# Kernel optimization log

Measured on AMD Instinct MI355X. Metric: run time of the kernel, lower is better.

Reference implementation:

```python
import jax, jax.numpy as jnp
import numpy as np

H = 128; R = 8; VN = 100; VA = 64
N = 8192; B = 64; L = 48; E = 65536


def setup_inputs() -> dict:
    key = jax.random.key(0)
    ks = jax.random.split(key, 24)
    s = 0.05
    nodeTypes = jax.random.randint(ks[0], (N,), 0, VN)
    edge_index = jax.random.randint(ks[1], (2, E), 0, N)
    edge_attr = jax.random.randint(ks[2], (E,), 0, R)
    bs = jnp.repeat(jnp.arange(B), N // B)              # sorted node->graph map
    nodes_bs = jnp.full((B,), N // B, dtype=jnp.int32)  # nodes per graph
    len_seq = jax.random.randint(ks[3], (B,), 1, L + 1).at[0].set(L)  # max == L
    sequence_input = (jax.random.uniform(ks[4], (N, L)) < 0.05).astype(jnp.float32)
    action_input = jax.random.randint(ks[5], (B,), 0, VA)
    params = dict(
        emb_nodes=jax.random.normal(ks[6], (VN, H)) * s,
        emb_actions=jax.random.normal(ks[7], (VA, H)) * s,
        rgcn_rel=jax.random.normal(ks[8], (3, R, H, H)) * s,   # per-layer relation weights
        rgcn_root=jax.random.normal(ks[9], (3, H, H)) * s,
        rgcn_bias=jnp.zeros((3, H)),
        gru_w_ih=jax.random.normal(ks[10], (3 * H, H)) * s,
        gru_w_hh=jax.random.normal(ks[11], (3 * H, H)) * s,
        gru_b_ih=jnp.zeros((3 * H,)),
        gru_b_hh=jnp.zeros((3 * H,)),
        linA_w=jax.random.normal(ks[12], (H, H)) * s,
        linA_b=jnp.zeros((H,)),
        linAf_w=jax.random.normal(ks[13], (VA, H)) * s,
        linAf_b=jnp.zeros((VA,)),
        linN_w=jax.random.normal(ks[14], (H, 2 * H)) * s,
        linN_b=jnp.zeros((H,)),
        linNf_w=jax.random.normal(ks[15], (1, H)) * s,
        linNf_b=jnp.zeros((1,)),
    )
    return dict(nodeTypes=nodeTypes, edge_index=edge_index, edge_attr=edge_attr,
                bs=bs, nodes_bs=nodes_bs, len_seq=len_seq,
                sequence_input=sequence_input, action_input=action_input, **params)


def reference(nodeTypes, edge_index, edge_attr, bs, nodes_bs, len_seq,
              sequence_input, action_input,
              emb_nodes, emb_actions, rgcn_rel, rgcn_root, rgcn_bias,
              gru_w_ih, gru_w_hh, gru_b_ih, gru_b_hh,
              linA_w, linA_b, linAf_w, linAf_b,
              linN_w, linN_b, linNf_w, linNf_b):
    n = nodeTypes.shape[0]
    b = nodes_bs.shape[0]
    h = emb_nodes.shape[1]
    r = rgcn_rel.shape[1]
    l = sequence_input.shape[1]

    x = emb_nodes[nodeTypes]                               # [N,H]
    src, dst = edge_index[0], edge_index[1]
    seg = dst * r + edge_attr                              # per (target, relation) segment
    cnt = jax.ops.segment_sum(jnp.ones((src.shape[0],), x.dtype), seg, n * r)
    denom = jnp.maximum(cnt, 1.0).reshape(n, r, 1)
    for li in range(3):
        agg = jax.ops.segment_sum(x[src], seg, n * r).reshape(n, r, h) / denom
        x = jax.nn.relu(jnp.einsum('nrh,rho->no', agg, rgcn_rel[li])
                        + x @ rgcn_root[li] + rgcn_bias[li])

    # global mean pool -> graph embedding
    h_G = jax.ops.segment_sum(x, bs, b) / nodes_bs[:, None].astype(x.dtype)  # [B,H]
    action = jax.nn.relu(h_G @ linA_w.T + linA_b) @ linAf_w.T + linAf_b      # [B,VA]

    sos = emb_actions[action_input][:, None, :]            # [B,1,H]
    # sequence embeddings: sum over nodes in each graph of seq[i,t]*x[i]
    emb_seq = sequence_input[:, :, None] * x[:, None, :]   # [N,L,H]
    out = jax.ops.segment_sum(emb_seq, bs, b)              # [B,L,H]
    input_gru = jnp.concatenate([sos, out], axis=1)[:, :l] # packed GRU only sees first L steps

    # single-layer GRU, h0 = h_G (torch gate order r,z,n)
    xW = input_gru @ gru_w_ih.T + gru_b_ih                 # [B,L,3H]
    def step(hprev, xw):
        hW = hprev @ gru_w_hh.T + gru_b_hh
        xr, xz, xn = jnp.split(xw, 3, -1)
        hr, hz, hn = jnp.split(hW, 3, -1)
        rg = jax.nn.sigmoid(xr + hr)
        zg = jax.nn.sigmoid(xz + hz)
        ng = jnp.tanh(xn + rg * hn)
        hnew = (1.0 - zg) * ng + zg * hprev
        return hnew, hnew
    _, hs = jax.lax.scan(step, h_G, jnp.swapaxes(xW, 0, 1))
    seq_out = jnp.swapaxes(hs, 0, 1)                       # [B,L,H]
    mask = jnp.arange(l)[None, :] < len_seq[:, None]       # pad_packed zero-pads
    seq_out = seq_out * mask[:, :, None]

    out_gru = seq_out[bs]                                  # repeat_interleave -> [N,L,H]
    concats = jnp.concatenate(
        [out_gru, jnp.broadcast_to(x[:, None, :], (n, l, h))], axis=2)  # [N,L,2H]
    hid = jax.nn.relu(concats @ linN_w.T + linN_b)         # [N,L,H]
    logits = (hid @ linNf_w.T + linNf_b)[..., 0]           # [N,L]

    # scatter_softmax over nodes grouped by graph (dim 0)
    m = jax.lax.stop_gradient(jax.ops.segment_max(logits, bs, b))
    e = jnp.exp(logits - m[bs])
    ssum = jax.ops.segment_sum(e, bs, b)
    nodes_final = e / ssum[bs]
    return action, nodes_final
```

## Files before the change

kernel.cpp:

```cpp
#include <hip/hip_runtime.h>
#include <hip/hip_bf16.h>

#define H   128
#define RR  8
#define NN  8192
#define BB  64
#define LL  48
#define EE  65536
#define NPG 128
#define VA  64
#define NSEG (NN*RR)
#define GPB 16

typedef unsigned short u16;
typedef unsigned int   u32;

__device__ __forceinline__ float b2f(u16 u) {
    union { u32 i; float f; } v; v.i = ((u32)u) << 16; return v.f;
}
__device__ __forceinline__ u16 f2b(float f) {
    union { float f; u32 i; } v; v.f = f;
    u32 x = v.i;
    return (u16)((x + 0x7fffu + ((x >> 16) & 1u)) >> 16);
}
__device__ __forceinline__ float2 up2(u32 p) {
    union { u32 i; float f; } a, b;
    a.i = p << 16; b.i = p & 0xffff0000u;
    return make_float2(a.f, b.f);
}
__device__ __forceinline__ u32 pk2(float a, float b) {
    return ((u32)f2b(b) << 16) | (u32)f2b(a);
}
__device__ __forceinline__ float rcpf(float x) { return __builtin_amdgcn_rcpf(x); }
__device__ __forceinline__ u32 cvtpk(float lo, float hi) {
    u32 r;
    asm("v_cvt_pk_bf16_f32 %0, %1, %2" : "=v"(r) : "v"(lo), "v"(hi));
    return r;
}

#define K_LOG2E  1.4426950408889634f
#define K_2LOG2E 2.8853900817779268f

typedef __attribute__((ext_vector_type(8))) short bf16x8;
typedef __attribute__((ext_vector_type(4))) float f32x4;
typedef __attribute__((ext_vector_type(4))) unsigned short u16x4;

__global__ __launch_bounds__(256) void k_prep(const int* __restrict__ nodeTypes,
                                              const float* __restrict__ emb_nodes,
                                              const float* __restrict__ rel,
                                              const float* __restrict__ root,
                                              const float* __restrict__ w_ih,
                                              float* __restrict__ x0,
                                              u16* __restrict__ WTt,
                                              u16* __restrict__ WTih,
                                              float* __restrict__ hGsum,
                                              int* __restrict__ fill) {
    int idx = blockIdx.x * 256 + threadIdx.x;
    if (idx < NSEG) fill[idx] = 0;
    if (idx < 384 * H) WTih[idx] = f2b(w_ih[idx]);
    if (idx < BB * H) hGsum[idx] = 0.f;
    if (idx < NN * H) {
        int n = idx >> 7, h = idx & (H - 1);
        x0[idx] = emb_nodes[(size_t)nodeTypes[n] * H + h];
    }
    int j = idx - NN * H;
    if (j < 0 || j >= 3 * 147456) return;
    int li  = j / 147456;
    int rem = j - li * 147456;
    int tile = rem / 36864;
    int r2   = rem - tile * 36864;
    int ks   = r2 / 1024;
    int r3   = r2 - ks * 1024;
    int sub  = r3 >> 9;
    int r4   = r3 & 511;
    int lane = r4 >> 3, jj = r4 & 7;
    int col = tile * 32 + sub * 16 + (lane & 15);
    int k   = ks * 32 + (lane >> 4) * 8 + jj;
    float v;
    if (k < 1024) v = rel[(((size_t)li * RR + (k >> 7)) * H + (k & 127)) * H + col];
    else          v = root[((size_t)li * H + (k - 1024)) * H + col];
    WTt[j] = f2b(v);
}

__global__ __launch_bounds__(256) void k_hist(const int* __restrict__ edge_index,
                                              const int* __restrict__ edge_attr,
                                              int* __restrict__ fill) {
    int e = blockIdx.x * 256 + threadIdx.x;
    if (e < EE) {
        int seg = edge_index[EE + e] * RR + edge_attr[e];
        atomicAdd(&fill[seg], 1);
    }
}

__global__ __launch_bounds__(256) void k_scan1(const int* __restrict__ fill,
                                               int* __restrict__ bsum) {
    __shared__ int red[4];
    int tid = threadIdx.x, lane = tid & 63, wv = tid >> 6;
    int v = fill[blockIdx.x * 256 + tid];
#pragma unroll
    for (int off = 32; off >= 1; off >>= 1) v += __shfl_down(v, off, 64);
    if (lane == 0) red[wv] = v;
    __syncthreads();
    if (tid == 0) bsum[blockIdx.x] = red[0] + red[1] + red[2] + red[3];
}

__global__ __launch_bounds__(256) void k_scan3(const int* __restrict__ bsum,
                                               int* __restrict__ fill,
                                               int* __restrict__ rowptr) {
    __shared__ int s[256], s2[256];
    __shared__ int boffs;
    int tid = threadIdx.x;
    int g = blockIdx.x * 256 + tid;
    int c = fill[g];
    int b0 = bsum[tid];
    s[tid] = c;
    s2[tid] = b0;
    __syncthreads();
    for (int off = 1; off < 256; off <<= 1) {
        int v  = (tid >= off) ? s[tid - off]  : 0;
        int v2 = (tid >= off) ? s2[tid - off] : 0;
        __syncthreads();
        s[tid] += v;
        s2[tid] += v2;
        __syncthreads();
    }
    if (blockIdx.x == 0 && tid == 255) rowptr[NSEG] = s2[255];
    if (tid == blockIdx.x) boffs = s2[tid] - b0;
    __syncthreads();
    int r = boffs + s[tid] - c;
    rowptr[g] = r;
    fill[g] = r;
}

__global__ __launch_bounds__(256) void k_scatter(const int* __restrict__ edge_index,
                                                 const int* __restrict__ edge_attr,
                                                 int* __restrict__ fill,
                                                 int* __restrict__ colidx) {
    int e = blockIdx.x * 256 + threadIdx.x;
    if (e < EE) {
        int seg = edge_index[EE + e] * RR + edge_attr[e];
        int pos = atomicAdd(&fill[seg], 1);
        colidx[pos] = edge_index[e];
    }
}

#define RGN 16
#define EPRE 512

__global__ __launch_bounds__(512) void k_rgcn(const float* __restrict__ xin,
                                              float* __restrict__ xout,
                                              const u16* __restrict__ WTt,
                                              const float* __restrict__ bias,
                                              const int* __restrict__ rowptr,
                                              const int* __restrict__ colidx,
                                              float* __restrict__ hGsum) {
    __shared__ u32 ab[RGN * 580];
    __shared__ int begs[RGN * RR + 1];
    __shared__ int eidx[EPRE];
    int tid = threadIdx.x, wv = tid >> 6, lane = tid & 63;
    int n0 = blockIdx.x * RGN, segbase = n0 * RR;

    if (tid <= RGN * RR) begs[tid] = rowptr[segbase + tid];
    __syncthreads();
    int E0 = begs[0], ne = begs[RGN * RR] - E0;
    for (int i = tid; i < ne && i < EPRE; i += 512) eidx[i] = colidx[E0 + i];
    __syncthreads();

    for (int s = wv; s < RGN * RR; s += 8) {
        int beg = begs[s], end = begs[s + 1];
        float a0 = 0.f, a1 = 0.f;
        for (int e = beg; e < end; ++e) {
            int off = e - E0;
            int src = (off < EPRE) ? eidx[off] : colidx[e];
            float2 v = ((const float2*)(xin + (size_t)src * H))[lane];
            a0 += v.x; a1 += v.y;
        }
        float inv = 1.f / fmaxf((float)(end - beg), 1.f);
        ab[(s >> 3) * 580 + ((s & 7) << 6) + lane] = pk2(a0 * inv, a1 * inv);
    }
    for (int i = wv; i < RGN; i += 8) {
        const float* xr = xin + (size_t)(n0 + i) * H + 2 * lane;
        ab[i * 580 + 512 + lane] = pk2(xr[0], xr[1]);
    }
    __syncthreads();

    int m = lane & 15, quad = lane >> 4;
    const u32* aP = ab + m * 580 + quad * 4;
    const u32* bT = (const u32*)WTt + (size_t)(wv >> 1) * 36 * 512 + (wv & 1) * 256 + lane * 4;
    f32x4 acc0 = {0.f, 0.f, 0.f, 0.f};
    bf16x8 b0c = *(const bf16x8*)bT;
    for (int ks = 0; ks < 36; ++ks) {
        bf16x8 b0n;
        if (ks < 35) b0n = *(const bf16x8*)(bT + (ks + 1) * 512);
        bf16x8 a = *(const bf16x8*)(aP + ks * 16);
        acc0 = __builtin_amdgcn_mfma_f32_16x16x32_bf16(a, b0c, acc0, 0, 0, 0);
        b0c = b0n;
    }
    int c0 = wv * 16 + m;
    float bv0 = bias[c0];
    float so0 = 0.f;
#pragma unroll
    for (int rg = 0; rg < 4; ++rg) {
        int n = n0 + quad * 4 + rg;
        float o0 = fmaxf(acc0[rg] + bv0, 0.f);
        xout[(size_t)n * H + c0] = o0;
        so0 += o0;
    }
    if (hGsum) {
        so0 += __shfl_xor(so0, 16, 64);
        so0 += __shfl_xor(so0, 32, 64);
        if (quad == 0) {
            int g = n0 >> 7;
            atomicAdd(&hGsum[g * H + c0], so0);
        }
    }
}

__global__ __launch_bounds__(256) void k_pool_seq(const float* __restrict__ hGsum,
                                                  const int* __restrict__ nodes_bs,
                                                  const float* __restrict__ linA_w,
                                                  const float* __restrict__ linA_b,
                                                  const float* __restrict__ linAf_w,
                                                  const float* __restrict__ linAf_b,
                                                  float* __restrict__ hG,
                                                  float* __restrict__ out,
                                                  const float* __restrict__ xf,
                                                  const float* __restrict__ seq,
                                                  const float* __restrict__ emb_actions,
                                                  const int* __restrict__ action_input,
                                                  float* __restrict__ igG) {
    __shared__ float xg[64][H];
    __shared__ u16 lists[LL][64];
    __shared__ int cnts[LL];
    int tid = threadIdx.x;

    if (blockIdx.x < BB) {
        float* hgs = &xg[0][0];
        float* t1  = &xg[1][0];
        int b = blockIdx.x, h = tid;
        if (h < H) {
            float hg = hGsum[(size_t)b * H + h] / (float)nodes_bs[b];
            hG[(size_t)b * H + h] = hg;
            hgs[h] = hg;
        }
        __syncthreads();
        if (h < H) {
            float acc = linA_b[h];
            const float* wr = linA_w + (size_t)h * H;
            for (int k = 0; k < H; ++k) acc += wr[k] * hgs[k];
            t1[h] = fmaxf(acc, 0.f);
        }
        __syncthreads();
        if (h < VA) {
            float a = linAf_b[h];
            const float* w2 = linAf_w + (size_t)h * H;
            for (int k = 0; k < H; ++k) a += w2[k] * t1[k];
            out[(size_t)b * VA + h] = a;
        }
        return;
    }

    int b = blockIdx.x - BB;
    int col = tid & 127, tg = tid >> 7;
    float acc[24];
#pragma unroll
    for (int m = 0; m < 24; ++m) acc[m] = 0.f;

    for (int chunk = 0; chunk < 2; ++chunk) {
        int i0 = b * NPG + chunk * 64;
        __syncthreads();
        if (tid < LL) cnts[tid] = 0;
        __syncthreads();
        for (int idx = tid; idx < 64 * H / 4; idx += 256)
            ((float4*)&xg[0][0])[idx] = ((const float4*)(xf + (size_t)i0 * H))[idx];
        for (int idx = tid; idx < 64 * LL; idx += 256) {
            int i = idx / LL, t = idx - i * LL;
            if (seq[(size_t)(i0 + i) * LL + t] != 0.f) {
                int p = atomicAdd(&cnts[t], 1);
                lists[t][p] = (u16)i;
            }
        }
        __syncthreads();
        for (int m = 0; m < 24; ++m) {
            int t = tg + 2 * m;
            int c = cnts[t];
            float a = acc[m];
            for (int p = 0; p < c; ++p) a += xg[lists[t][p]][col];
            acc[m] = a;
        }
    }
    if (tid < H)
        igG[((size_t)b * LL) * H + tid] = emb_actions[(size_t)action_input[b] * H + tid];
#pragma unroll
    for (int m = 0; m < 24; ++m) {
        int t = tg + 2 * m;
        if (t < LL - 1)
            igG[((size_t)b * LL + t + 1) * H + col] = acc[m];
    }
}

__global__ __launch_bounds__(256) void k_xw(const float* __restrict__ igG,
                                            const u16* __restrict__ WTih,
                                            const float* __restrict__ b_ih,
                                            const float* __restrict__ b_hh,
                                            u16* __restrict__ xwG) {
    __shared__ u32 ab[16 * 68];
    int tid = threadIdx.x, wv = tid >> 6, lane = tid & 63;
    int n0 = blockIdx.x * 16;
    for (int s = tid; s < 16 * 64; s += 256) {
        int row = s >> 6, kp = s & 63;
        float2 v = *(const float2*)(igG + (size_t)(n0 + row) * H + 2 * kp);
        ab[row * 68 + kp] = pk2(v.x, v.y);
    }
    __syncthreads();
    int m = lane & 15, quad = lane >> 4;
    const u32* aP = ab + m * 68 + quad * 4;
    f32x4 acc[6];
#pragma unroll
    for (int i = 0; i < 6; ++i) acc[i] = (f32x4){0.f, 0.f, 0.f, 0.f};
#pragma unroll
    for (int ks = 0; ks < 4; ++ks) {
        bf16x8 a = *(const bf16x8*)(aP + ks * 16);
#pragma unroll
        for (int tc = 0; tc < 6; ++tc) {
            int colr = wv * 96 + tc * 16 + m;
            bf16x8 bfr = *(const bf16x8*)((const u32*)WTih + (size_t)colr * 64 + quad * 4 + ks * 16);
            acc[tc] = __builtin_amdgcn_mfma_f32_16x16x32_bf16(a, bfr, acc[tc], 0, 0, 0);
        }
    }
#pragma unroll
    for (int tc = 0; tc < 6; ++tc) {
        int c = wv * 96 + tc * 16 + m;
        float bv = b_ih[c] + ((c < 256) ? b_hh[c] : 0.f);
        float sc = (c < 256) ? K_LOG2E : K_2LOG2E;
        int R = c & 127, gate = c >> 7;
#pragma unroll
        for (int rg = 0; rg < 4; ++rg) {
            int r = n0 + quad * 4 + rg;
            int bb = r / 48, tt = r - bb * 48;
            size_t o = (((((size_t)(bb >> 4) * LL + tt) * 8 + (R >> 4)) * 3 + gate) * 256)
                     + (((R >> 2) & 3) << 6) + ((bb & 15) << 2) + (R & 3);
            xwG[o] = f2b((acc[tc][rg] + bv) * sc);
        }
    }
}

#define GRU_BLKS 4
#define BX_BLKS  (NN / 32)
#define SMEM_BYTES 33024

__global__ __launch_bounds__(512) void k_gru_bx(const u16* __restrict__ xw2,
                                                const float* __restrict__ hG,
                                                const float* __restrict__ w_hh,
                                                const float* __restrict__ b_hh,
                                                const int* __restrict__ len_seq,
                                                float* __restrict__ soutG,
                                                const float* __restrict__ xf,
                                                const float* __restrict__ linN_w,
                                                const float* __restrict__ linN_b,
                                                u16* __restrict__ BxU) {
    __shared__ __align__(16) char smem[SMEM_BYTES];
    int tid = threadIdx.x;

    if (blockIdx.x >= GRU_BLKS) {
        float* xl = (float*)smem;
        float* wb = (float*)(smem + 16384);
        int bid = blockIdx.x - GRU_BLKS;
        int n0 = bid * 32;
        for (int idx = tid; idx < 32 * H; idx += 512)
            xl[idx] = xf[(size_t)n0 * H + idx];
        int col = tid & 127, g = tid >> 7;
        float bv = linN_b[col];
        float acc[8] = {bv, bv, bv, bv, bv, bv, bv, bv};
        for (int c = 0; c < 4; ++c) {
            int k0 = c * 32;
            __syncthreads();
            for (int idx = tid; idx < 32 * H; idx += 512) {
                int r = idx >> 5, kk = idx & 31;
                wb[kk * 130 + r] = linN_w[(size_t)r * (2 * H) + H + k0 + kk];
            }
            __syncthreads();
#pragma unroll
            for (int kk = 0; kk < 32; ++kk) {
                float w = wb[kk * 130 + col];
#pragma unroll
                for (int j = 0; j < 8; ++j) acc[j] += xl[(g * 8 + j) * H + k0 + kk] * w;
            }
        }
#pragma unroll
        for (int j = 0; j < 8; ++j)
            BxU[(size_t)(n0 + g * 8 + j) * H + col] = f2b(acc[j]);
        return;
    }

    u16* hA = (u16*)smem;
    int lane = tid & 63, wv = tid >> 6;
    int mi = lane & 15, quad = lane >> 4;
    int gblk = blockIdx.x;
    int g_abs = gblk * GPB + mi;
    int R0 = 16 * wv + 4 * quad;

    int eW = (((wv >> 1) * 64) + (mi + 16 * ((2 * wv + (quad >> 1)) & 3))) * 8
             + 4 * (quad & 1);

    bf16x8 wfr[3][4];
#pragma unroll
    for (int gate = 0; gate < 3; ++gate) {
        int T = wv + 8 * gate;
        float sc = (gate == 2) ? K_2LOG2E : K_LOG2E;
#pragma unroll
        for (int ks = 0; ks < 4; ++ks) {
            const float* wp = w_hh + (size_t)(16 * T + mi) * H + quad * 8 + ks * 32;
            float4 f0 = *(const float4*)wp;
            float4 f1 = *(const float4*)(wp + 4);
            bf16x8 v;
            v[0] = (short)f2b(f0.x * sc); v[1] = (short)f2b(f0.y * sc);
            v[2] = (short)f2b(f0.z * sc); v[3] = (short)f2b(f0.w * sc);
            v[4] = (short)f2b(f1.x * sc); v[5] = (short)f2b(f1.y * sc);
            v[6] = (short)f2b(f1.z * sc); v[7] = (short)f2b(f1.w * sc);
            wfr[gate][ks] = v;
        }
    }
    float4 bn = *(const float4*)(b_hh + 256 + R0);
    float4 h0 = *(const float4*)(hG + (size_t)g_abs * H + R0);
    int ls = len_seq[g_abs];

    float hp[4]  = {h0.x, h0.y, h0.z, h0.w};
    float bnn[4] = {bn.x * K_2LOG2E, bn.y * K_2LOG2E, bn.z * K_2LOG2E, bn.w * K_2LOG2E};

    auto storeh = [&](int buf, const float* hv) {
        u32 w0 = cvtpk(hv[0], hv[1]);
        u32 w1 = cvtpk(hv[2], hv[3]);
        *(uint2*)&hA[buf * 2048 + eW] = make_uint2(w0, w1);
    };
    auto loadxw = [&](int t, u16x4* d) {
        const u16* p = xw2 + ((((size_t)gblk * LL + t) * 8 + wv) * 3) * 256
                     + (quad << 6) + (mi << 2);
        d[0] = *(const u16x4*)(p);
        d[1] = *(const u16x4*)(p + 256);
        d[2] = *(const u16x4*)(p + 512);
    };

    auto step = [&](int t, const u16x4* x, int buf) {
        f32x4 acc[3];
        acc[0] = (f32x4){0.f, 0.f, 0.f, 0.f};
        acc[1] = (f32x4){0.f, 0.f, 0.f, 0.f};
        acc[2] = (f32x4){bnn[0], bnn[1], bnn[2], bnn[3]};
#pragma unroll
        for (int ks = 0; ks < 4; ++ks) {
            const int e = (ks * 64 + lane) * 8;
            bf16x8 bh = *(const bf16x8*)&hA[buf * 2048 + e];
#pragma unroll
            for (int gate = 0; gate < 3; ++gate)
                acc[gate] = __builtin_amdgcn_mfma_f32_16x16x32_bf16(wfr[gate][ks], bh, acc[gate], 0, 0, 0);
        }
        float hv[4];
        float4 so;
#pragma unroll
        for (int r = 0; r < 4; ++r) {
            float xr = b2f(x[0][r]);
            float xz = b2f(x[1][r]);
            float xn = b2f(x[2][r]);
            float rg = rcpf(1.f + __builtin_amdgcn_exp2f(-(xr + acc[0][r])));
            float zg = rcpf(1.f + __builtin_amdgcn_exp2f(-(xz + acc[1][r])));
            float u  = xn + rg * acc[2][r];
            float ng = 1.f - 2.f * rcpf(__builtin_amdgcn_exp2f(u) + 1.f);
            float hn = ng + zg * (hp[r] - ng);
            hp[r] = hn;
            hv[r] = hn;
            ((float*)&so)[r] = (t < ls) ? hn : 0.f;
        }
        *(float4*)(soutG + ((size_t)g_abs * LL + t) * H + R0) = so;
        storeh(buf ^ 1, hv);
    };

    u16x4 xa[3], xb[3];
    loadxw(0, xa);
    loadxw(1, xb);
    storeh(0, hp);
    asm volatile("s_waitcnt lgkmcnt(0)\n\ts_barrier" ::: "memory");

    for (int t = 0; t < LL; t += 2) {
        step(t, xa, 0);
        if (t + 2 < LL) loadxw(t + 2, xa);
        asm volatile("s_waitcnt lgkmcnt(0)\n\ts_barrier" ::: "memory");
        step(t + 1, xb, 1);
        if (t + 3 < LL) loadxw(t + 3, xb);
        asm volatile("s_waitcnt lgkmcnt(0)\n\ts_barrier" ::: "memory");
    }
}

__global__ __launch_bounds__(256) void k_a2(const float* __restrict__ soutG,
                                            const float* __restrict__ linN_w,
                                            float* __restrict__ A2) {
    __shared__ float wb[32][130];
    __shared__ float xl[16][H];
    int tid = threadIdx.x;
    int n0 = blockIdx.x * 16;
    for (int idx = tid; idx < 16 * H; idx += 256)
        xl[idx >> 7][idx & 127] = soutG[(size_t)n0 * H + idx];
    int col = tid & 127, g = tid >> 7;
    float acc[8] = {0.f, 0.f, 0.f, 0.f, 0.f, 0.f, 0.f, 0.f};
    for (int c = 0; c < 4; ++c) {
        int k0 = c * 32;
        __syncthreads();
        for (int idx = tid; idx < 32 * H; idx += 256) {
            int r = idx >> 5, kk = idx & 31;
            wb[kk][r] = linN_w[(size_t)r * (2 * H) + k0 + kk];
        }
        __syncthreads();
#pragma unroll
        for (int kk = 0; kk < 32; ++kk) {
            float w = wb[kk][col];
#pragma unroll
            for (int j = 0; j < 8; ++j) acc[j] += xl[g * 8 + j][k0 + kk] * w;
        }
    }
#pragma unroll
    for (int j = 0; j < 8; ++j)
        A2[(size_t)(n0 + g * 8 + j) * H + col] = acc[j];
}

__global__ __launch_bounds__(256) void k_logits(const float* __restrict__ A2,
                                                const u16* __restrict__ BxU,
                                                const float* __restrict__ linNf_w,
                                                float* __restrict__ logits) {
    __shared__ float a2s[LL][130];
    __shared__ float bxs[16][130];
    __shared__ float w2s[H];
    int tid = threadIdx.x;
    int g = blockIdx.x >> 3, tile = blockIdx.x & 7;
    int n0g = g * NPG + tile * 16;

    for (int i2 = tid; i2 < LL * 64; i2 += 256) {
        int r = i2 >> 6, c2 = i2 & 63;
        *(float2*)&a2s[r][2 * c2] = *(const float2*)(A2 + ((size_t)g * LL + r) * H + 2 * c2);
    }
    for (int iu = tid; iu < 16 * 64; iu += 256) {
        int r = iu >> 6, c = iu & 63;
        float2 v = up2(((const u32*)BxU)[(size_t)(n0g + r) * 64 + c]);
        *(float2*)&bxs[r][2 * c] = v;
    }
    if (tid < H) w2s[tid] = linNf_w[tid];
    __syncthreads();

    int n = tid & 15, tt = tid >> 4;
#pragma unroll
    for (int pass = 0; pass < 3; ++pass) {
        int t = tt + 16 * pass;
        float acc = 0.f;
#pragma unroll
        for (int kp = 0; kp < 64; ++kp) {
            float2 a2 = *(const float2*)&a2s[t][2 * kp];
            float2 bx = *(const float2*)&bxs[n][2 * kp];
            float2 w  = *(const float2*)&w2s[2 * kp];
            acc += w.x * fmaxf(a2.x + bx.x, 0.f) + w.y * fmaxf(a2.y + bx.y, 0.f);
        }
        logits[(size_t)(n0g + n) * LL + t] = acc;
    }
}

__global__ __launch_bounds__(256) void k_softmax(const float* __restrict__ logits,
                                                 float* __restrict__ out) {
    __shared__ float lg[NPG][LL + 1];
    __shared__ float pm[4][LL], ps[4][LL];
    __shared__ float mv[LL], inv[LL];
    int b = blockIdx.x, tid = threadIdx.x;
    int n0 = b * NPG;
    for (int idx = tid; idx < NPG * LL; idx += 256) {
        int n = idx / LL, t = idx - n * LL;
        lg[n][t] = logits[(size_t)n0 * LL + idx];
    }
    __syncthreads();
    int t = tid & 63, seg = tid >> 6;
    if (t < LL) {
        float m = -1e30f;
        int nb = seg * 32;
        for (int n = nb; n < nb + 32; ++n) m = fmaxf(m, lg[n][t]);
        pm[seg][t] = m;
    }
    __syncthreads();
    if (tid < LL)
        mv[tid] = fmaxf(fmaxf(pm[0][tid], pm[1][tid]), fmaxf(pm[2][tid], pm[3][tid]));
    __syncthreads();
    if (t < LL) {
        float m = mv[t], s = 0.f;
        int nb = seg * 32;
        for (int n = nb; n < nb + 32; ++n) {
            float e = __expf(lg[n][t] - m);
            lg[n][t] = e;
            s += e;
        }
        ps[seg][t] = s;
    }
    __syncthreads();
    if (tid < LL)
        inv[tid] = 1.f / (ps[0][tid] + ps[1][tid] + ps[2][tid] + ps[3][tid]);
    __syncthreads();
    for (int idx = tid; idx < NPG * LL; idx += 256) {
        int n = idx / LL, tc = idx - n * LL;
        out[(size_t)BB * VA + (size_t)n0 * LL + idx] = lg[n][tc] * inv[tc];
    }
}

extern "C" void kernel_launch(void* const* d_in, const int* in_sizes, int n_in,
                              void* d_out, int out_size, void* d_ws, size_t ws_size,
                              hipStream_t stream) {
    (void)in_sizes; (void)n_in; (void)out_size; (void)ws_size;
    const int*   nodeTypes    = (const int*)d_in[0];
    const int*   edge_index   = (const int*)d_in[1];
    const int*   edge_attr    = (const int*)d_in[2];
    const int*   nodes_bs     = (const int*)d_in[4];
    const int*   len_seq      = (const int*)d_in[5];
    const float* seq_in       = (const float*)d_in[6];
    const int*   action_input = (const int*)d_in[7];
    const float* emb_nodes    = (const float*)d_in[8];
    const float* emb_actions  = (const float*)d_in[9];
    const float* rgcn_rel     = (const float*)d_in[10];
    const float* rgcn_root    = (const float*)d_in[11];
    const float* rgcn_bias    = (const float*)d_in[12];
    const float* gru_w_ih     = (const float*)d_in[13];
    const float* gru_w_hh     = (const float*)d_in[14];
    const float* gru_b_ih     = (const float*)d_in[15];
    const float* gru_b_hh     = (const float*)d_in[16];
    const float* linA_w       = (const float*)d_in[17];
    const float* linA_b       = (const float*)d_in[18];
    const float* linAf_w      = (const float*)d_in[19];
    const float* linAf_b      = (const float*)d_in[20];
    const float* linN_w       = (const float*)d_in[21];
    const float* linN_b       = (const float*)d_in[22];
    const float* linNf_w      = (const float*)d_in[23];

    char* w = (char*)d_ws;
    float* x0      = (float*)(w + 0);
    u16*   xwG     = (u16*)  (w + 0);
    float* logitsW = (float*)(w + 0);
    float* soutG   = (float*)(w + 2359296);
    float* x1      = (float*)(w + 4194304);
    float* igG     = (float*)(w + 8388608);
    float* A2      = (float*)(w + 8388608);
    u16*   BxU     = (u16*)  (w + 9961472);
    int*   bsum    = (int*)  (w + 9961472);
    float* hGsum   = (float*)(w + 9969664);
    int*   rowptr  = (int*)  (w + 11567104);
    int*   fill    = (int*)  (w + 11829760);
    float* hG      = (float*)(w + 12058624);
    int*   colidx  = (int*)  (w + 12091904);
    u16*   WTih    = (u16*)  (w + 12354048);
    u16*   WT      = (u16*)  (w + 12616192);

    float* out_f = (float*)d_out;

    k_prep<<<dim3(5824), dim3(256), 0, stream>>>(nodeTypes, emb_nodes, rgcn_rel,
        rgcn_root, gru_w_ih, x0, WT, WTih, hGsum, fill);
    k_hist<<<dim3(256), dim3(256), 0, stream>>>(edge_index, edge_attr, fill);
    k_scan1<<<dim3(256), dim3(256), 0, stream>>>(fill, bsum);
    k_scan3<<<dim3(256), dim3(256), 0, stream>>>(bsum, fill, rowptr);
    k_scatter<<<dim3(256), dim3(256), 0, stream>>>(edge_index, edge_attr, fill, colidx);

    const int rg_grid = NN / RGN;
    k_rgcn<<<dim3(rg_grid), dim3(512), 0, stream>>>(x0, x1,
        WT + 0 * 147456, rgcn_bias + 0 * H, rowptr, colidx, nullptr);
    k_rgcn<<<dim3(rg_grid), dim3(512), 0, stream>>>(x1, x0,
        WT + 1 * 147456, rgcn_bias + 1 * H, rowptr, colidx, nullptr);
    k_rgcn<<<dim3(rg_grid), dim3(512), 0, stream>>>(x0, x1,
        WT + 2 * 147456, rgcn_bias + 2 * H, rowptr, colidx, hGsum);

    k_pool_seq<<<dim3(2 * BB), dim3(256), 0, stream>>>(hGsum, nodes_bs, linA_w, linA_b,
        linAf_w, linAf_b, hG, out_f, x1, seq_in, emb_actions, action_input, igG);
    k_xw<<<dim3(BB * LL / 16), dim3(256), 0, stream>>>(igG, WTih, gru_b_ih, gru_b_hh, xwG);
    k_gru_bx<<<dim3(GRU_BLKS + BX_BLKS), dim3(512), 0, stream>>>(xwG, hG, gru_w_hh,
        gru_b_hh, len_seq, soutG, x1, linN_w, linN_b, BxU);
    k_a2<<<dim3(BB * LL / 16), dim3(256), 0, stream>>>(soutG, linN_w, A2);
    k_logits<<<dim3(BB * 8), dim3(256), 0, stream>>>(A2, BxU, linNf_w, logitsW);
    k_softmax<<<dim3(BB), dim3(256), 0, stream>>>(logitsW, out_f);
}
```

Before: 309.1 us.

## Fuse CSR build into cooperative kernel and merge logits with softmax

Result: slower. 478.0 us (+54.7%).

```diff
diff --git a/kernel.cpp b/kernel.cpp
--- a/kernel.cpp
+++ b/kernel.cpp
@@ -1,5 +1,8 @@
 #include <hip/hip_runtime.h>
 #include <hip/hip_bf16.h>
+#include <hip/hip_cooperative_groups.h>
+
+namespace cg = cooperative_groups;
 
 #define H   128
 #define RR  8
@@ -82,63 +85,59 @@
     WTt[j] = f2b(v);
 }
 
-__global__ __launch_bounds__(256) void k_hist(const int* __restrict__ edge_index,
-                                              const int* __restrict__ edge_attr,
-                                              int* __restrict__ fill) {
-    int e = blockIdx.x * 256 + threadIdx.x;
-    if (e < EE) {
-        int seg = edge_index[EE + e] * RR + edge_attr[e];
-        atomicAdd(&fill[seg], 1);
-    }
-}
-
-__global__ __launch_bounds__(256) void k_scan1(const int* __restrict__ fill,
-                                               int* __restrict__ bsum) {
+__global__ __launch_bounds__(256) void k_csr(const int* __restrict__ edge_index,
+                                             const int* __restrict__ edge_attr,
+                                             int* __restrict__ fill,
+                                             int* __restrict__ bsum,
+                                             int* __restrict__ rowptr,
+                                             int* __restrict__ colidx) {
+    cg::grid_group grid = cg::this_grid();
+    __shared__ int s[256], s2[256];
     __shared__ int red[4];
-    int tid = threadIdx.x, lane = tid & 63, wv = tid >> 6;
-    int v = fill[blockIdx.x * 256 + tid];
-#pragma unroll
-    for (int off = 32; off >= 1; off >>= 1) v += __shfl_down(v, off, 64);
-    if (lane == 0) red[wv] = v;
-    __syncthreads();
-    if (tid == 0) bsum[blockIdx.x] = red[0] + red[1] + red[2] + red[3];
-}
-
-__global__ __launch_bounds__(256) void k_scan3(const int* __restrict__ bsum,
-                                               int* __restrict__ fill,
-                                               int* __restrict__ rowptr) {
-    __shared__ int s[256], s2[256];
     __shared__ int boffs;
     int tid = threadIdx.x;
-    int g = blockIdx.x * 256 + tid;
-    int c = fill[g];
-    int b0 = bsum[tid];
-    s[tid] = c;
-    s2[tid] = b0;
-    __syncthreads();
-    for (int off = 1; off < 256; off <<= 1) {
-        int v  = (tid >= off) ? s[tid - off]  : 0;
-        int v2 = (tid >= off) ? s2[tid - off] : 0;
-        __syncthreads();
-        s[tid] += v;
-        s2[tid] += v2;
-        __syncthreads();
-    }
-    if (blockIdx.x == 0 && tid == 255) rowptr[NSEG] = s2[255];
-    if (tid == blockIdx.x) boffs = s2[tid] - b0;
-    __syncthreads();
-    int r = boffs + s[tid] - c;
-    rowptr[g] = r;
-    fill[g] = r;
-}
-
-__global__ __launch_bounds__(256) void k_scatter(const int* __restrict__ edge_index,
-                                                 const int* __restrict__ edge_attr,
-                                                 int* __restrict__ fill,
-                                                 int* __restrict__ colidx) {
-    int e = blockIdx.x * 256 + threadIdx.x;
-    if (e < EE) {
-        int seg = edge_index[EE + e] * RR + edge_attr[e];
+    int e = blockIdx.x * 256 + tid;
+    int seg = edge_index[EE + e] * RR + edge_attr[e];
+
+    atomicAdd(&fill[seg], 1);
+    grid.sync();
+
+    {
+        int lane = tid & 63, wv = tid >> 6;
+        int v = fill[blockIdx.x * 256 + tid];
+#pragma unroll
+        for (int off = 32; off >= 1; off >>= 1) v += __shfl_down(v, off, 64);
+        if (lane == 0) red[wv] = v;
+        __syncthreads();
+        if (tid == 0) bsum[blockIdx.x] = red[0] + red[1] + red[2] + red[3];
+    }
+    grid.sync();
+
+    {
+        int g = blockIdx.x * 256 + tid;
+        int c = fill[g];
+        int b0 = bsum[tid];
+        s[tid] = c;
+        s2[tid] = b0;
+        __syncthreads();
+        for (int off = 1; off < 256; off <<= 1) {
+            int v  = (tid >= off) ? s[tid - off]  : 0;
+            int v2 = (tid >= off) ? s2[tid - off] : 0;
+            __syncthreads();
+            s[tid] += v;
+            s2[tid] += v2;
+            __syncthreads();
+        }
+        if (blockIdx.x == 0 && tid == 255) rowptr[NSEG] = s2[255];
+        if (tid == blockIdx.x) boffs = s2[tid] - b0;
+        __syncthreads();
+        int r = boffs + s[tid] - c;
+        rowptr[g] = r;
+        fill[g] = r;
+    }
+    grid.sync();
+
+    {
         int pos = atomicAdd(&fill[seg], 1);
         colidx[pos] = edge_index[e];
     }
@@ -521,62 +520,56 @@
         A2[(size_t)(n0 + g * 8 + j) * H + col] = acc[j];
 }
 
-__global__ __launch_bounds__(256) void k_logits(const float* __restrict__ A2,
-                                                const u16* __restrict__ BxU,
-                                                const float* __restrict__ linNf_w,
-                                                float* __restrict__ logits) {
+__global__ __launch_bounds__(256) void k_lsm(const float* __restrict__ A2,
+                                             const u16* __restrict__ BxU,
+                                             const float* __restrict__ linNf_w,
+                                             float* __restrict__ out) {
     __shared__ float a2s[LL][130];
     __shared__ float bxs[16][130];
     __shared__ float w2s[H];
+    __shared__ float lg[NPG][LL + 1];
+    __shared__ float pm[4][LL], ps[4][LL];
+    __shared__ float mv[LL], inv[LL];
     int tid = threadIdx.x;
-    int g = blockIdx.x >> 3, tile = blockIdx.x & 7;
-    int n0g = g * NPG + tile * 16;
+    int g = blockIdx.x;
 
     for (int i2 = tid; i2 < LL * 64; i2 += 256) {
         int r = i2 >> 6, c2 = i2 & 63;
         *(float2*)&a2s[r][2 * c2] = *(const float2*)(A2 + ((size_t)g * LL + r) * H + 2 * c2);
     }
-    for (int iu = tid; iu < 16 * 64; iu += 256) {
-        int r = iu >> 6, c = iu & 63;
-        float2 v = up2(((const u32*)BxU)[(size_t)(n0g + r) * 64 + c]);
-        *(float2*)&bxs[r][2 * c] = v;
-    }
     if (tid < H) w2s[tid] = linNf_w[tid];
-    __syncthreads();
 
     int n = tid & 15, tt = tid >> 4;
-#pragma unroll
-    for (int pass = 0; pass < 3; ++pass) {
-        int t = tt + 16 * pass;
-        float acc = 0.f;
-#pragma unroll
-        for (int kp = 0; kp < 64; ++kp) {
-            float2 a2 = *(const float2*)&a2s[t][2 * kp];
-            float2 bx = *(const float2*)&bxs[n][2 * kp];
-            float2 w  = *(const float2*)&w2s[2 * kp];
-            acc += w.x * fmaxf(a2.x + bx.x, 0.f) + w.y * fmaxf(a2.y + bx.y, 0.f);
-        }
-        logits[(size_t)(n0g + n) * LL + t] = acc;
-    }
-}
-
-__global__ __launch_bounds__(256) void k_softmax(const float* __restrict__ logits,
-                                                 float* __restrict__ out) {
-    __shared__ float lg[NPG][LL + 1];
-    __shared__ float pm[4][LL], ps[4][LL];
-    __shared__ float mv[LL], inv[LL];
-    int b = blockIdx.x, tid = threadIdx.x;
-    int n0 = b * NPG;
-    for (int idx = tid; idx < NPG * LL; idx += 256) {
-        int n = idx / LL, t = idx - n * LL;
-        lg[n][t] = logits[(size_t)n0 * LL + idx];
-    }
-    __syncthreads();
+    for (int tile = 0; tile < 8; ++tile) {
+        int n0g = g * NPG + tile * 16;
+        __syncthreads();
+        for (int iu = tid; iu < 16 * 64; iu += 256) {
+            int r = iu >> 6, c = iu & 63;
+            float2 v = up2(((const u32*)BxU)[(size_t)(n0g + r) * 64 + c]);
+            *(float2*)&bxs[r][2 * c] = v;
+        }
+        __syncthreads();
+#pragma unroll
+        for (int pass = 0; pass < 3; ++pass) {
+            int t = tt + 16 * pass;
+            float acc = 0.f;
+#pragma unroll
+            for (int kp = 0; kp < 64; ++kp) {
+                float2 a2 = *(const float2*)&a2s[t][2 * kp];
+                float2 bx = *(const float2*)&bxs[n][2 * kp];
+                float2 w  = *(const float2*)&w2s[2 * kp];
+                acc += w.x * fmaxf(a2.x + bx.x, 0.f) + w.y * fmaxf(a2.y + bx.y, 0.f);
+            }
+            lg[tile * 16 + n][t] = acc;
+        }
+    }
+    __syncthreads();
+
     int t = tid & 63, seg = tid >> 6;
     if (t < LL) {
         float m = -1e30f;
         int nb = seg * 32;
-        for (int n = nb; n < nb + 32; ++n) m = fmaxf(m, lg[n][t]);
+        for (int nn = nb; nn < nb + 32; ++nn) m = fmaxf(m, lg[nn][t]);
         pm[seg][t] = m;
     }
     __syncthreads();
@@ -586,9 +579,9 @@
     if (t < LL) {
         float m = mv[t], s = 0.f;
         int nb = seg * 32;
-        for (int n = nb; n < nb + 32; ++n) {
-            float e = __expf(lg[n][t] - m);
-            lg[n][t] = e;
+        for (int nn = nb; nn < nb + 32; ++nn) {
+            float e = __expf(lg[nn][t] - m);
+            lg[nn][t] = e;
             s += e;
         }
         ps[seg][t] = s;
@@ -598,8 +591,8 @@
         inv[tid] = 1.f / (ps[0][tid] + ps[1][tid] + ps[2][tid] + ps[3][tid]);
     __syncthreads();
     for (int idx = tid; idx < NPG * LL; idx += 256) {
-        int n = idx / LL, tc = idx - n * LL;
-        out[(size_t)BB * VA + (size_t)n0 * LL + idx] = lg[n][tc] * inv[tc];
+        int nn = idx / LL, tc = idx - nn * LL;
+        out[(size_t)BB * VA + (size_t)g * NPG * LL + idx] = lg[nn][tc] * inv[tc];
     }
 }
 
@@ -634,7 +627,6 @@
     char* w = (char*)d_ws;
     float* x0      = (float*)(w + 0);
     u16*   xwG     = (u16*)  (w + 0);
-    float* logitsW = (float*)(w + 0);
     float* soutG   = (float*)(w + 2359296);
     float* x1      = (float*)(w + 4194304);
     float* igG     = (float*)(w + 8388608);
@@ -653,10 +645,12 @@
 
     k_prep<<<dim3(5824), dim3(256), 0, stream>>>(nodeTypes, emb_nodes, rgcn_rel,
         rgcn_root, gru_w_ih, x0, WT, WTih, hGsum, fill);
-    k_hist<<<dim3(256), dim3(256), 0, stream>>>(edge_index, edge_attr, fill);
-    k_scan1<<<dim3(256), dim3(256), 0, stream>>>(fill, bsum);
-    k_scan3<<<dim3(256), dim3(256), 0, stream>>>(bsum, fill, rowptr);
-    k_scatter<<<dim3(256), dim3(256), 0, stream>>>(edge_index, edge_attr, fill, colidx);
+
+    {
+        void* args[] = { (void*)&edge_index, (void*)&edge_attr, (void*)&fill,
+                         (void*)&bsum, (void*)&rowptr, (void*)&colidx };
+        hipLaunchCooperativeKernel((void*)k_csr, dim3(256), dim3(256), args, 0, stream);
+    }
 
     const int rg_grid = NN / RGN;
     k_rgcn<<<dim3(rg_grid), dim3(512), 0, stream>>>(x0, x1,
@@ -672,6 +666,5 @@
     k_gru_bx<<<dim3(GRU_BLKS + BX_BLKS), dim3(512), 0, stream>>>(xwG, hG, gru_w_hh,
         gru_b_hh, len_seq, soutG, x1, linN_w, linN_b, BxU);
     k_a2<<<dim3(BB * LL / 16), dim3(256), 0, stream>>>(soutG, linN_w, A2);
-    k_logits<<<dim3(BB * 8), dim3(256), 0, stream>>>(A2, BxU, linNf_w, logitsW);
-    k_softmax<<<dim3(BB), dim3(256), 0, stream>>>(logitsW, out_f);
-}
+    k_lsm<<<dim3(BB), dim3(256), 0, stream>>>(A2, BxU, linNf_w, out_f);
+}
```
